# Optimization experiments

Measured on AMD Instinct MI355X. Metric: run time of the kernel, lower is better.

The kernel has to match this reference:

```python
import jax, jax.numpy as jnp
import numpy as np

N_STFT = 513
N_BARKS = 128
SAMPLE_RATE = 16000
F_MIN = 0.0
F_MAX = 8000.0
MAX_ITER = 30
TOL_LOSS = 1e-5
TOL_CHANGE = 1e-8
LR = 0.1
MOMENTUM = 0.9
BATCH = 4
TIME = 512


def _hz_to_bark(f):
    # traunmuller scale
    b = 26.81 * f / (1960.0 + f) - 0.53
    b = jnp.where(b < 2.0, b + 0.15 * (2.0 - b), b)
    b = jnp.where(b > 20.1, b + 0.22 * (b - 20.1), b)
    return b


def _bark_to_hz(b):
    b = jnp.where(b < 2.0, (b - 0.3) / 0.85, b)
    b = jnp.where(b > 20.1, (b + 4.422) / 1.22, b)
    return 1960.0 * (b + 0.53) / (26.28 - b)


def barkscale_fbanks():
    all_freqs = jnp.linspace(0.0, float(SAMPLE_RATE // 2), N_STFT)
    b_min = _hz_to_bark(jnp.float32(F_MIN))
    b_max = _hz_to_bark(jnp.float32(F_MAX))
    b_pts = jnp.linspace(b_min, b_max, N_BARKS + 2)
    f_pts = _bark_to_hz(b_pts)
    f_diff = f_pts[1:] - f_pts[:-1]                  # (n_barks+1,)
    slopes = f_pts[None, :] - all_freqs[:, None]     # (freq, n_barks+2)
    down = -slopes[:, :-2] / f_diff[:-1]
    up = slopes[:, 2:] / f_diff[1:]
    return jnp.maximum(0.0, jnp.minimum(down, up))   # (freq, n_barks)


def setup_inputs() -> dict:
    key = jax.random.key(0)
    k1, k2 = jax.random.split(key)
    barkspec = jax.random.uniform(k1, (BATCH, N_BARKS, TIME), dtype=jnp.float32)
    fb = barkscale_fbanks().astype(jnp.float32)                 # (freq, n_barks)
    spec_init = jax.random.uniform(k2, (BATCH, TIME, N_STFT), dtype=jnp.float32)
    return {"barkspec": barkspec, "fb": fb, "spec_init": spec_init}


def reference(barkspec, fb, spec_init):
    B, K, T = barkspec.shape
    m = jnp.swapaxes(barkspec, -1, -2)          # (B, T, n_barks)
    inv_n = 1.0 / (B * T)

    def step(carry, _):
        spec, buf, prev_loss, done = carry
        diff = m - jnp.einsum('btf,fk->btk', spec, fb)          # (B, T, K)
        loss = (diff * diff).sum(-1).mean()
        # closed-form grad of mean_{b,t} sum_k diff^2 wrt spec
        grad = (-2.0 * inv_n) * jnp.einsum('btk,fk->btf', diff, fb)
        # torch SGD with momentum, no dampening/nesterov
        buf_n = MOMENTUM * buf + grad
        spec_n = jnp.maximum(spec - LR * buf_n, 0.0)            # clamp(min=0)
        stop = (loss < TOL_LOSS) | (jnp.abs(prev_loss - loss) < TOL_CHANGE)
        spec = jnp.where(done, spec, spec_n)
        buf = jnp.where(done, buf, buf_n)
        prev = jnp.where(done, prev_loss, loss)
        return (spec, buf, prev, done | stop), None

    init = (spec_init, jnp.zeros_like(spec_init), jnp.float32(jnp.inf),
            jnp.array(False))
    (spec, _, _, _), _ = jax.lax.scan(step, init, None, length=MAX_ITER)
    return jnp.swapaxes(spec, -1, -2)           # (B, freq, T)
```

## Files before the change

### kernel.cpp

```cpp
#include <hip/hip_runtime.h>


#define NSTFT 513
#define NBARK 128
#define BATCH 4
#define TIME  512
#define MAXIT 30
#define NROWS (BATCH*TIME)
#define SA 6
#define SB 20

#define WS_S_OFF   0
#define WS_FT_OFF  256
#define WS_HA_OFF  8464
#define WS_HB_OFF  8976
#define WS_WT_OFF  9488
#define WS_BP_OFF  22800

__global__ __launch_bounds__(64) void setup_taps(const float* __restrict__ fb,
                                                 char* __restrict__ ws) {
    const int f = blockIdx.x, lane = threadIdx.x;
    const float2 v = ((const float2*)(fb + (size_t)f * NBARK))[lane];
    unsigned long long mx = __ballot(v.x > 0.f);
    unsigned long long my = __ballot(v.y > 0.f);
    int kx = mx ? 2 * (__ffsll(mx) - 1)     : 999;
    int ky = my ? 2 * (__ffsll(my) - 1) + 1 : 999;
    int k1 = min(kx, ky);
    float w1 = 0.f, w2 = 0.f;
    if (k1 < NBARK) {
        float sx = __shfl(v.x, k1 >> 1);
        float sy = __shfl(v.y, k1 >> 1);
        w1 = (k1 & 1) ? sy : sx;
        const int k2 = k1 + 1;
        if (k2 < NBARK) {
            float tx = __shfl(v.x, k2 >> 1);
            float ty = __shfl(v.y, k2 >> 1);
            w2 = (k2 & 1) ? ty : tx;
        }
    } else {
        k1 = (f < 256) ? 0 : 127;
    }
    if (lane == 0) {
        float4 e;
        e.x = __int_as_float(k1); e.y = w1;
        e.z = 0.f;                e.w = w2;
        ((float4*)(ws + WS_FT_OFF))[f] = e;
    }
}

__global__ __launch_bounds__(64) void setup_lanes(char* __restrict__ ws) {
    const int c = blockIdx.x, lane = threadIdx.x;
    const float4* ftab = (const float4*)(ws + WS_FT_OFF);
    int fmin = 0x7fffffff, fmax = -1;
    float4 e9[9];
#pragma unroll
    for (int s = 0; s < 9; ++s) {
        int f = lane + 64*s;
        e9[s] = (f < NSTFT) ? ftab[f] : make_float4(__int_as_float(-1),0,0,0);
        if (f < NSTFT && __float_as_int(e9[s].x) == c) {
            fmin = min(fmin, f); fmax = max(fmax, f);
        }
    }
#pragma unroll
    for (int m = 32; m; m >>= 1) {
        fmin = min(fmin, __shfl_xor(fmin, m));
        fmax = max(fmax, __shfl_xor(fmax, m));
    }
    int cnt = (fmax >= 0) ? (fmax - fmin + 1) : 0;
    if (fmax < 0) fmin = 0;
    const int cap  = (c < 64) ? SA : SB;
    const int base = (c < 64) ? 0  : SA;
    const int lf   = (c < 64) ? c  : 127 - c;
    cnt = min(cnt, cap);
    if (lane == 0)
        ((int2*)(ws + (c < 64 ? WS_HA_OFF : WS_HB_OFF)))[lf] =
            make_int2(fmin, cnt);
    if (lane < cap) {
        float2 wv = make_float2(0.f, 0.f);
        if (lane < cnt) {
            float4 e = ftab[fmin + lane];
            wv = make_float2(e.y, e.w);
        }
        ((float2*)(ws + WS_WT_OFF))[(base + lane)*64 + lf] = wv;
    }
}

__global__ __launch_bounds__(64, 2) void
iter_kernel(const float* __restrict__ barkspec,
            const float* __restrict__ spec_init,
            float* __restrict__ out,
            char* __restrict__ ws, int mode)
{
    const int lane = threadIdx.x;

    int niter = MAXIT;
    if (mode) {
        int S = *(const volatile int*)(ws + WS_S_OFF);
        if (S >= MAXIT) return;
        niter = S;
    }

    const int r     = blockIdx.x;
    const int batch = r >> 9;
    const int t     = r & (TIME - 1);

    const int2 hA = ((const int2*)(ws + WS_HA_OFF))[lane];
    const int2 hB = ((const int2*)(ws + WS_HB_OFF))[lane];
    const float2* wt = (const float2*)(ws + WS_WT_OFF);
    const float* spg = spec_init + ((size_t)batch*TIME + t)*NSTFT;

    float w1A[SA], w2A[SA], spA[SA], bfA[SA];
    float w1B[SB], w2B[SB], spB[SB], bfB[SB];
#pragma unroll
    for (int i = 0; i < SA; ++i) {
        float2 v = wt[i*64 + lane];
        w1A[i] = v.x; w2A[i] = v.y;
        spA[i] = (i < hA.y) ? spg[hA.x + i] : 0.f;
        bfA[i] = 0.f;
    }
#pragma unroll
    for (int i = 0; i < SB; ++i) {
        float2 v = wt[(SA + i)*64 + lane];
        w1B[i] = v.x; w2B[i] = v.y;
        spB[i] = (i < hB.y) ? spg[hB.x + i] : 0.f;
        bfB[i] = 0.f;
    }

    const float* bs = barkspec + (size_t)batch*NBARK*TIME + t;
    const float m0 = bs[(size_t)lane*TIME];
    const float m1 = bs[(size_t)(127 - lane)*TIME];

    float* bp = (float*)(ws + WS_BP_OFF);
    const float GC = -2.0f / (float)NROWS;

    float lp_prev = 0.f;

#pragma unroll 2
    for (int it = 0; it < niter; ++it) {
        float sBA = 0.f, sBB = 0.f;
#pragma unroll
        for (int i = 0; i < SA; ++i) sBA = fmaf(spA[i], w2A[i], sBA);
#pragma unroll
        for (int i = 0; i < SB; ++i) sBB = fmaf(spB[i], w2B[i], sBB);
        float cAin = __shfl_up(sBA, 1);
        float cBin = __shfl_down(sBB, 1);

        if (!mode && it > 0) {
            float lp = lp_prev;
#pragma unroll
            for (int m = 32; m; m >>= 1) lp += __shfl_xor(lp, m);
            if (lane == 0) bp[(it - 1)*NROWS + r] = lp;
        }

        float sAA = 0.f, sAB = 0.f;
#pragma unroll
        for (int i = 0; i < SA; ++i) sAA = fmaf(spA[i], w1A[i], sAA);
#pragma unroll
        for (int i = 0; i < SB; ++i) sAB = fmaf(spB[i], w1B[i], sAB);

        if (lane == 0)  cAin = 0.f;
        if (lane == 63) cBin = sBA;
        const float d0 = m0 - (sAA + cAin);
        const float d1 = m1 - (sAB + cBin);
        lp_prev = fmaf(d0, d0, d1*d1);

        float dAn = __shfl_down(d0, 1);
        float dBn = __shfl_up(d1, 1);
        const float g0 = GC * d0, g1 = GC * d1;
#pragma unroll
        for (int i = 0; i < SA; ++i) bfA[i] *= 0.9f;
#pragma unroll
        for (int i = 0; i < SB; ++i) bfB[i] *= 0.9f;
        if (lane == 63) dAn = d1;
        const float gA = GC * dAn, gB = GC * dBn;
#pragma unroll
        for (int i = 0; i < SA; ++i) {
            float g = fmaf(g0, w1A[i], gA * w2A[i]);
            bfA[i] += g;
            float v = fmaf(-0.1f, bfA[i], spA[i]);
            spA[i] = v < 0.f ? 0.f : v;
        }
#pragma unroll
        for (int i = 0; i < SB; ++i) {
            float g = fmaf(g1, w1B[i], gB * w2B[i]);
            bfB[i] += g;
            float v = fmaf(-0.1f, bfB[i], spB[i]);
            spB[i] = v < 0.f ? 0.f : v;
        }
    }

    if (!mode) {
        float lp = lp_prev;
#pragma unroll
        for (int m = 32; m; m >>= 1) lp += __shfl_xor(lp, m);
        if (lane == 0) bp[(niter - 1)*NROWS + r] = lp;
    }

    float* og = out + ((size_t)batch*NSTFT)*TIME + t;
#pragma unroll
    for (int i = 0; i < SA; ++i)
        if (i < hA.y) og[(size_t)(hA.x + i)*TIME] = spA[i];
#pragma unroll
    for (int i = 0; i < SB; ++i)
        if (i < hB.y) og[(size_t)(hB.x + i)*TIME] = spB[i];
}

__global__ __launch_bounds__(1024) void scan_all(char* __restrict__ ws) {
    __shared__ float losses[MAXIT];
    const int tid = threadIdx.x, wave = tid >> 6, lane = tid & 63;
    const float* bp = (const float*)(ws + WS_BP_OFF);
    for (int it = wave; it < MAXIT; it += 16) {
        const float4* b4 = (const float4*)(bp + (size_t)it*NROWS);
        float s = 0.f;
#pragma unroll
        for (int j = 0; j < NROWS/256; ++j) {
            float4 v = b4[j*64 + lane];
            s += (v.x + v.y) + (v.z + v.w);
        }
#pragma unroll
        for (int m = 32; m; m >>= 1) s += __shfl_xor(s, m);
        if (lane == 0) losses[it] = s * (1.0f/(float)NROWS);
    }
    __syncthreads();
    if (tid == 0) {
        float prev = __builtin_inff();
        int S = MAXIT;
        for (int i = 0; i < MAXIT; ++i) {
            float l = losses[i];
            if (l < 1e-5f || fabsf(prev - l) < 1e-8f) { S = i + 1; break; }
            prev = l;
        }
        *(int*)(ws + WS_S_OFF) = S;
    }
}

extern "C" void kernel_launch(void* const* d_in, const int* in_sizes, int n_in,
                              void* d_out, int out_size, void* d_ws, size_t ws_size,
                              hipStream_t stream)
{
    const float* barkspec  = (const float*)d_in[0];
    const float* fb        = (const float*)d_in[1];
    const float* spec_init = (const float*)d_in[2];
    float* out = (float*)d_out;
    char* ws = (char*)d_ws;

    setup_taps <<<NSTFT, 64, 0, stream>>>(fb, ws);
    setup_lanes<<<NBARK, 64, 0, stream>>>(ws);
    iter_kernel<<<NROWS, 64, 0, stream>>>(barkspec, spec_init, out, ws, 0);
    scan_all   <<<1, 1024, 0, stream>>>(ws);
    iter_kernel<<<NROWS, 64, 0, stream>>>(barkspec, spec_init, out, ws, 1);
}
```

Before: 104.9 us.

## Snapshot spectra every iteration and select the stop-step output instead of re-running

The main kernel now stores each row's spectrum to a workspace snapshot after every one of the 30 iterations, instead of writing the final output directly. The second iteration pass, which previously recomputed up to the early-stop step, is replaced by a select_out kernel that copies the snapshot for the chosen step into the transposed output. This removes the possible recomputation when early stopping triggers. In exchange it writes roughly 127 MB of snapshots per call and adds an extra transpose-copy kernel, even though the recompute pass exits immediately when no early stop occurs. The loop's unroll-by-2 pragma is also dropped.

```diff
diff --git a/kernel.cpp b/kernel.cpp
--- a/kernel.cpp
+++ b/kernel.cpp
@@ -9,13 +9,15 @@
 #define NROWS (BATCH*TIME)
 #define SA 6
 #define SB 20
-
-#define WS_S_OFF   0
-#define WS_FT_OFF  256
-#define WS_HA_OFF  8464
-#define WS_HB_OFF  8976
-#define WS_WT_OFF  9488
-#define WS_BP_OFF  22800
+#define ROWF 516
+
+#define WS_S_OFF    0
+#define WS_FT_OFF   256
+#define WS_HA_OFF   8464
+#define WS_HB_OFF   8976
+#define WS_WT_OFF   9488
+#define WS_BP_OFF   22800
+#define WS_SNAP_OFF 268800
 
 __global__ __launch_bounds__(64) void setup_taps(const float* __restrict__ fb,
                                                  char* __restrict__ ws) {
@@ -52,13 +54,12 @@
     const int c = blockIdx.x, lane = threadIdx.x;
     const float4* ftab = (const float4*)(ws + WS_FT_OFF);
     int fmin = 0x7fffffff, fmax = -1;
-    float4 e9[9];
 #pragma unroll
     for (int s = 0; s < 9; ++s) {
         int f = lane + 64*s;
-        e9[s] = (f < NSTFT) ? ftab[f] : make_float4(__int_as_float(-1),0,0,0);
-        if (f < NSTFT && __float_as_int(e9[s].x) == c) {
-            fmin = min(fmin, f); fmax = max(fmax, f);
+        if (f < NSTFT) {
+            float4 e = ftab[f];
+            if (__float_as_int(e.x) == c) { fmin = min(fmin, f); fmax = max(fmax, f); }
         }
     }
 #pragma unroll
@@ -86,19 +87,11 @@
 }
 
 __global__ __launch_bounds__(64, 2) void
-iter_kernel(const float* __restrict__ barkspec,
-            const float* __restrict__ spec_init,
-            float* __restrict__ out,
-            char* __restrict__ ws, int mode)
+iter_snap(const float* __restrict__ barkspec,
+          const float* __restrict__ spec_init,
+          char* __restrict__ ws)
 {
     const int lane = threadIdx.x;
-
-    int niter = MAXIT;
-    if (mode) {
-        int S = *(const volatile int*)(ws + WS_S_OFF);
-        if (S >= MAXIT) return;
-        niter = S;
-    }
 
     const int r     = blockIdx.x;
     const int batch = r >> 9;
@@ -131,12 +124,14 @@
     const float m1 = bs[(size_t)(127 - lane)*TIME];
 
     float* bp = (float*)(ws + WS_BP_OFF);
+    float* snA = (float*)(ws + WS_SNAP_OFF) + (size_t)r*ROWF + hA.x;
+    float* snB = (float*)(ws + WS_SNAP_OFF) + (size_t)r*ROWF + hB.x;
+    const size_t SNAP_IT = (size_t)NROWS * ROWF;
+
     const float GC = -2.0f / (float)NROWS;
-
     float lp_prev = 0.f;
 
-#pragma unroll 2
-    for (int it = 0; it < niter; ++it) {
+    for (int it = 0; it < MAXIT; ++it) {
         float sBA = 0.f, sBB = 0.f;
 #pragma unroll
         for (int i = 0; i < SA; ++i) sBA = fmaf(spA[i], w2A[i], sBA);
@@ -145,7 +140,7 @@
         float cAin = __shfl_up(sBA, 1);
         float cBin = __shfl_down(sBB, 1);
 
-        if (!mode && it > 0) {
+        if (it > 0) {
             float lp = lp_prev;
 #pragma unroll
             for (int m = 32; m; m >>= 1) lp += __shfl_xor(lp, m);
@@ -187,22 +182,22 @@
             float v = fmaf(-0.1f, bfB[i], spB[i]);
             spB[i] = v < 0.f ? 0.f : v;
         }
-    }
-
-    if (!mode) {
+
+#pragma unroll
+        for (int i = 0; i < SA; ++i)
+            if (i < hA.y) snA[i] = spA[i];
+#pragma unroll
+        for (int i = 0; i < SB; ++i)
+            if (i < hB.y) snB[i] = spB[i];
+        snA += SNAP_IT; snB += SNAP_IT;
+    }
+
+    {
         float lp = lp_prev;
 #pragma unroll
         for (int m = 32; m; m >>= 1) lp += __shfl_xor(lp, m);
-        if (lane == 0) bp[(niter - 1)*NROWS + r] = lp;
-    }
-
-    float* og = out + ((size_t)batch*NSTFT)*TIME + t;
-#pragma unroll
-    for (int i = 0; i < SA; ++i)
-        if (i < hA.y) og[(size_t)(hA.x + i)*TIME] = spA[i];
-#pragma unroll
-    for (int i = 0; i < SB; ++i)
-        if (i < hB.y) og[(size_t)(hB.x + i)*TIME] = spB[i];
+        if (lane == 0) bp[(MAXIT - 1)*NROWS + r] = lp;
+    }
 }
 
 __global__ __launch_bounds__(1024) void scan_all(char* __restrict__ ws) {
@@ -231,6 +226,26 @@
             prev = l;
         }
         *(int*)(ws + WS_S_OFF) = S;
+    }
+}
+
+__global__ __launch_bounds__(64) void select_out(const char* __restrict__ ws,
+                                                 float* __restrict__ out) {
+    const int lane = threadIdx.x;
+    const int S = *(const int*)(ws + WS_S_OFF);
+    const float* snap = (const float*)(ws + WS_SNAP_OFF)
+                      + (size_t)(S - 1) * NROWS * ROWF;
+    const int b  = blockIdx.x / 129;
+    const int f0 = (blockIdx.x % 129) * 4;
+    float* og = out + ((size_t)b*NSTFT + f0)*TIME;
+    for (int t0 = 0; t0 < TIME; t0 += 64) {
+        const int t = t0 + lane;
+        const int r = (b << 9) | t;
+        float4 v = *(const float4*)(snap + (size_t)r*ROWF + f0);
+        og[t] = v.x;
+        if (f0 + 1 < NSTFT) og[(size_t)TIME   + t] = v.y;
+        if (f0 + 2 < NSTFT) og[(size_t)2*TIME + t] = v.z;
+        if (f0 + 3 < NSTFT) og[(size_t)3*TIME + t] = v.w;
     }
 }
 
@@ -246,7 +261,7 @@
 
     setup_taps <<<NSTFT, 64, 0, stream>>>(fb, ws);
     setup_lanes<<<NBARK, 64, 0, stream>>>(ws);
-    iter_kernel<<<NROWS, 64, 0, stream>>>(barkspec, spec_init, out, ws, 0);
+    iter_snap  <<<NROWS, 64, 0, stream>>>(barkspec, spec_init, ws);
     scan_all   <<<1, 1024, 0, stream>>>(ws);
-    iter_kernel<<<NROWS, 64, 0, stream>>>(barkspec, spec_init, out, ws, 1);
-}
+    select_out <<<BATCH*129, 64, 0, stream>>>(ws, out);
+}
```

Result: slower. 170.4 us (+62.5%).

## Checkpoint optimizer state periodically and replay only the remaining iterations

Applied to the files above, without the earlier changes.

The first iteration kernel now always runs all 30 steps without writing the output. After steps 8, 16 and 24 it saves each row's spectrum and momentum registers to workspace. A new repair kernel reads the stop iteration S, restores the nearest checkpoint (or the initial state) and replays only the remaining steps before writing the output. The aim is to cap the redundant recompute for early stopping at fewer than eight iterations. In exchange it writes roughly 80 MB of checkpoints, and it always launches a repair pass that reloads state and reruns up to six steps, even when S is 30 and the old code could exit immediately.

```diff
diff --git a/kernel.cpp b/kernel.cpp
--- a/kernel.cpp
+++ b/kernel.cpp
@@ -9,6 +9,7 @@
 #define NROWS (BATCH*TIME)
 #define SA 6
 #define SB 20
+#define CPF  ((SA+SB)*64)
 
 #define WS_S_OFF   0
 #define WS_FT_OFF  256
@@ -16,6 +17,7 @@
 #define WS_HB_OFF  8976
 #define WS_WT_OFF  9488
 #define WS_BP_OFF  22800
+#define WS_CP_OFF  268800
 
 __global__ __launch_bounds__(64) void setup_taps(const float* __restrict__ fb,
                                                  char* __restrict__ ws) {
@@ -52,13 +54,12 @@
     const int c = blockIdx.x, lane = threadIdx.x;
     const float4* ftab = (const float4*)(ws + WS_FT_OFF);
     int fmin = 0x7fffffff, fmax = -1;
-    float4 e9[9];
 #pragma unroll
     for (int s = 0; s < 9; ++s) {
         int f = lane + 64*s;
-        e9[s] = (f < NSTFT) ? ftab[f] : make_float4(__int_as_float(-1),0,0,0);
-        if (f < NSTFT && __float_as_int(e9[s].x) == c) {
-            fmin = min(fmin, f); fmax = max(fmax, f);
+        if (f < NSTFT) {
+            float4 e = ftab[f];
+            if (__float_as_int(e.x) == c) { fmin = min(fmin, f); fmax = max(fmax, f); }
         }
     }
 #pragma unroll
@@ -86,20 +87,11 @@
 }
 
 __global__ __launch_bounds__(64, 2) void
-iter_kernel(const float* __restrict__ barkspec,
-            const float* __restrict__ spec_init,
-            float* __restrict__ out,
-            char* __restrict__ ws, int mode)
+iter_cp(const float* __restrict__ barkspec,
+        const float* __restrict__ spec_init,
+        char* __restrict__ ws)
 {
     const int lane = threadIdx.x;
-
-    int niter = MAXIT;
-    if (mode) {
-        int S = *(const volatile int*)(ws + WS_S_OFF);
-        if (S >= MAXIT) return;
-        niter = S;
-    }
-
     const int r     = blockIdx.x;
     const int batch = r >> 9;
     const int t     = r & (TIME - 1);
@@ -131,12 +123,11 @@
     const float m1 = bs[(size_t)(127 - lane)*TIME];
 
     float* bp = (float*)(ws + WS_BP_OFF);
+    float* cp = (float*)(ws + WS_CP_OFF);
     const float GC = -2.0f / (float)NROWS;
-
     float lp_prev = 0.f;
 
-#pragma unroll 2
-    for (int it = 0; it < niter; ++it) {
+    for (int it = 0; it < MAXIT; ++it) {
         float sBA = 0.f, sBB = 0.f;
 #pragma unroll
         for (int i = 0; i < SA; ++i) sBA = fmaf(spA[i], w2A[i], sBA);
@@ -145,7 +136,7 @@
         float cAin = __shfl_up(sBA, 1);
         float cBin = __shfl_down(sBB, 1);
 
-        if (!mode && it > 0) {
+        if (it > 0) {
             float lp = lp_prev;
 #pragma unroll
             for (int m = 32; m; m >>= 1) lp += __shfl_xor(lp, m);
@@ -187,22 +178,28 @@
             float v = fmaf(-0.1f, bfB[i], spB[i]);
             spB[i] = v < 0.f ? 0.f : v;
         }
-    }
-
-    if (!mode) {
+
+        if (it == 7 || it == 15 || it == 23) {
+            const int c = it >> 3;
+            float* cs = cp + ((size_t)(c*2 + 0)*NROWS + r)*CPF + lane;
+            float* cb = cp + ((size_t)(c*2 + 1)*NROWS + r)*CPF + lane;
+#pragma unroll
+            for (int i = 0; i < SA; ++i) {
+                cs[i*64] = spA[i];  cb[i*64] = bfA[i];
+            }
+#pragma unroll
+            for (int i = 0; i < SB; ++i) {
+                cs[(SA + i)*64] = spB[i];  cb[(SA + i)*64] = bfB[i];
+            }
+        }
+    }
+
+    {
         float lp = lp_prev;
 #pragma unroll
         for (int m = 32; m; m >>= 1) lp += __shfl_xor(lp, m);
-        if (lane == 0) bp[(niter - 1)*NROWS + r] = lp;
-    }
-
-    float* og = out + ((size_t)batch*NSTFT)*TIME + t;
-#pragma unroll
-    for (int i = 0; i < SA; ++i)
-        if (i < hA.y) og[(size_t)(hA.x + i)*TIME] = spA[i];
-#pragma unroll
-    for (int i = 0; i < SB; ++i)
-        if (i < hB.y) og[(size_t)(hB.x + i)*TIME] = spB[i];
+        if (lane == 0) bp[(MAXIT - 1)*NROWS + r] = lp;
+    }
 }
 
 __global__ __launch_bounds__(1024) void scan_all(char* __restrict__ ws) {
@@ -232,6 +229,122 @@
         }
         *(int*)(ws + WS_S_OFF) = S;
     }
+}
+
+__global__ __launch_bounds__(64) void
+repair_out(const float* __restrict__ barkspec,
+           const float* __restrict__ spec_init,
+           float* __restrict__ out,
+           const char* __restrict__ ws)
+{
+    const int lane = threadIdx.x;
+    const int r     = blockIdx.x;
+    const int batch = r >> 9;
+    const int t     = r & (TIME - 1);
+
+    const int S    = *(const int*)(ws + WS_S_OFF);
+    const int base = (S >= 24) ? 24 : (S >= 16) ? 16 : (S >= 8) ? 8 : 0;
+    const int R    = S - base;
+
+    const int2 hA = ((const int2*)(ws + WS_HA_OFF))[lane];
+    const int2 hB = ((const int2*)(ws + WS_HB_OFF))[lane];
+    const float2* wt = (const float2*)(ws + WS_WT_OFF);
+
+    float w1A[SA], w2A[SA], spA[SA], bfA[SA];
+    float w1B[SB], w2B[SB], spB[SB], bfB[SB];
+#pragma unroll
+    for (int i = 0; i < SA; ++i) {
+        float2 v = wt[i*64 + lane];
+        w1A[i] = v.x; w2A[i] = v.y;
+    }
+#pragma unroll
+    for (int i = 0; i < SB; ++i) {
+        float2 v = wt[(SA + i)*64 + lane];
+        w1B[i] = v.x; w2B[i] = v.y;
+    }
+
+    if (base == 0) {
+        const float* spg = spec_init + ((size_t)batch*TIME + t)*NSTFT;
+#pragma unroll
+        for (int i = 0; i < SA; ++i) {
+            spA[i] = (i < hA.y) ? spg[hA.x + i] : 0.f;  bfA[i] = 0.f;
+        }
+#pragma unroll
+        for (int i = 0; i < SB; ++i) {
+            spB[i] = (i < hB.y) ? spg[hB.x + i] : 0.f;  bfB[i] = 0.f;
+        }
+    } else {
+        const int c = (base >> 3) - 1;
+        const float* cp = (const float*)(ws + WS_CP_OFF);
+        const float* cs = cp + ((size_t)(c*2 + 0)*NROWS + r)*CPF + lane;
+        const float* cb = cp + ((size_t)(c*2 + 1)*NROWS + r)*CPF + lane;
+#pragma unroll
+        for (int i = 0; i < SA; ++i) {
+            spA[i] = cs[i*64];  bfA[i] = cb[i*64];
+        }
+#pragma unroll
+        for (int i = 0; i < SB; ++i) {
+            spB[i] = cs[(SA + i)*64];  bfB[i] = cb[(SA + i)*64];
+        }
+    }
+
+    const float* bs = barkspec + (size_t)batch*NBARK*TIME + t;
+    const float m0 = bs[(size_t)lane*TIME];
+    const float m1 = bs[(size_t)(127 - lane)*TIME];
+    const float GC = -2.0f / (float)NROWS;
+
+    for (int it = 0; it < R; ++it) {
+        float sBA = 0.f, sBB = 0.f;
+#pragma unroll
+        for (int i = 0; i < SA; ++i) sBA = fmaf(spA[i], w2A[i], sBA);
+#pragma unroll
+        for (int i = 0; i < SB; ++i) sBB = fmaf(spB[i], w2B[i], sBB);
+        float cAin = __shfl_up(sBA, 1);
+        float cBin = __shfl_down(sBB, 1);
+
+        float sAA = 0.f, sAB = 0.f;
+#pragma unroll
+        for (int i = 0; i < SA; ++i) sAA = fmaf(spA[i], w1A[i], sAA);
+#pragma unroll
+        for (int i = 0; i < SB; ++i) sAB = fmaf(spB[i], w1B[i], sAB);
+
+        if (lane == 0)  cAin = 0.f;
+        if (lane == 63) cBin = sBA;
+        const float d0 = m0 - (sAA + cAin);
+        const float d1 = m1 - (sAB + cBin);
+
+        float dAn = __shfl_down(d0, 1);
+        float dBn = __shfl_up(d1, 1);
+        const float g0 = GC * d0, g1 = GC * d1;
+#pragma unroll
+        for (int i = 0; i < SA; ++i) bfA[i] *= 0.9f;
+#pragma unroll
+        for (int i = 0; i < SB; ++i) bfB[i] *= 0.9f;
+        if (lane == 63) dAn = d1;
+        const float gA = GC * dAn, gB = GC * dBn;
+#pragma unroll
+        for (int i = 0; i < SA; ++i) {
+            float g = fmaf(g0, w1A[i], gA * w2A[i]);
+            bfA[i] += g;
+            float v = fmaf(-0.1f, bfA[i], spA[i]);
+            spA[i] = v < 0.f ? 0.f : v;
+        }
+#pragma unroll
+        for (int i = 0; i < SB; ++i) {
+            float g = fmaf(g1, w1B[i], gB * w2B[i]);
+            bfB[i] += g;
+            float v = fmaf(-0.1f, bfB[i], spB[i]);
+            spB[i] = v < 0.f ? 0.f : v;
+        }
+    }
+
+    float* og = out + ((size_t)batch*NSTFT)*TIME + t;
+#pragma unroll
+    for (int i = 0; i < SA; ++i)
+        if (i < hA.y) og[(size_t)(hA.x + i)*TIME] = spA[i];
+#pragma unroll
+    for (int i = 0; i < SB; ++i)
+        if (i < hB.y) og[(size_t)(hB.x + i)*TIME] = spB[i];
 }
 
 extern "C" void kernel_launch(void* const* d_in, const int* in_sizes, int n_in,
@@ -246,7 +359,7 @@
 
     setup_taps <<<NSTFT, 64, 0, stream>>>(fb, ws);
     setup_lanes<<<NBARK, 64, 0, stream>>>(ws);
-    iter_kernel<<<NROWS, 64, 0, stream>>>(barkspec, spec_init, out, ws, 0);
+    iter_cp    <<<NROWS, 64, 0, stream>>>(barkspec, spec_init, ws);
     scan_all   <<<1, 1024, 0, stream>>>(ws);
-    iter_kernel<<<NROWS, 64, 0, stream>>>(barkspec, spec_init, out, ws, 1);
-}
+    repair_out <<<NROWS, 64, 0, stream>>>(barkspec, spec_init, out, ws);
+}
```

Measured after the change: 121.2 us. 1.16x slower.

## Store per-lane losses, reduce in a multi-block kernel, scan in iter kernel

Applied to the files above, without the earlier changes.

Each iteration now writes per-lane squared errors straight to workspace, so the per-iteration wave shuffle reduction in the solver loop goes away. The single-block scan is replaced by a 30-block reduce kernel that sums each iteration's losses in parallel. The stop-iteration scan moves into the second solver pass, where every block recomputes it. The dot products are split into two accumulators to shorten dependency chains. The price is 64x more loss traffic to memory (about 15 MB written and then read back).

```diff
diff --git a/kernel.cpp b/kernel.cpp
--- a/kernel.cpp
+++ b/kernel.cpp
@@ -10,12 +10,12 @@
 #define SA 6
 #define SB 20
 
-#define WS_S_OFF   0
+#define WS_L_OFF   16
 #define WS_FT_OFF  256
 #define WS_HA_OFF  8464
 #define WS_HB_OFF  8976
 #define WS_WT_OFF  9488
-#define WS_BP_OFF  22800
+#define WS_BP_OFF  22848
 
 __global__ __launch_bounds__(64) void setup_taps(const float* __restrict__ fb,
                                                  char* __restrict__ ws) {
@@ -52,13 +52,12 @@
     const int c = blockIdx.x, lane = threadIdx.x;
     const float4* ftab = (const float4*)(ws + WS_FT_OFF);
     int fmin = 0x7fffffff, fmax = -1;
-    float4 e9[9];
 #pragma unroll
     for (int s = 0; s < 9; ++s) {
         int f = lane + 64*s;
-        e9[s] = (f < NSTFT) ? ftab[f] : make_float4(__int_as_float(-1),0,0,0);
-        if (f < NSTFT && __float_as_int(e9[s].x) == c) {
-            fmin = min(fmin, f); fmax = max(fmax, f);
+        if (f < NSTFT) {
+            float4 e = ftab[f];
+            if (__float_as_int(e.x) == c) { fmin = min(fmin, f); fmax = max(fmax, f); }
         }
     }
 #pragma unroll
@@ -95,134 +94,7 @@
 
     int niter = MAXIT;
     if (mode) {
-        int S = *(const volatile int*)(ws + WS_S_OFF);
-        if (S >= MAXIT) return;
-        niter = S;
-    }
-
-    const int r     = blockIdx.x;
-    const int batch = r >> 9;
-    const int t     = r & (TIME - 1);
-
-    const int2 hA = ((const int2*)(ws + WS_HA_OFF))[lane];
-    const int2 hB = ((const int2*)(ws + WS_HB_OFF))[lane];
-    const float2* wt = (const float2*)(ws + WS_WT_OFF);
-    const float* spg = spec_init + ((size_t)batch*TIME + t)*NSTFT;
-
-    float w1A[SA], w2A[SA], spA[SA], bfA[SA];
-    float w1B[SB], w2B[SB], spB[SB], bfB[SB];
-#pragma unroll
-    for (int i = 0; i < SA; ++i) {
-        float2 v = wt[i*64 + lane];
-        w1A[i] = v.x; w2A[i] = v.y;
-        spA[i] = (i < hA.y) ? spg[hA.x + i] : 0.f;
-        bfA[i] = 0.f;
-    }
-#pragma unroll
-    for (int i = 0; i < SB; ++i) {
-        float2 v = wt[(SA + i)*64 + lane];
-        w1B[i] = v.x; w2B[i] = v.y;
-        spB[i] = (i < hB.y) ? spg[hB.x + i] : 0.f;
-        bfB[i] = 0.f;
-    }
-
-    const float* bs = barkspec + (size_t)batch*NBARK*TIME + t;
-    const float m0 = bs[(size_t)lane*TIME];
-    const float m1 = bs[(size_t)(127 - lane)*TIME];
-
-    float* bp = (float*)(ws + WS_BP_OFF);
-    const float GC = -2.0f / (float)NROWS;
-
-    float lp_prev = 0.f;
-
-#pragma unroll 2
-    for (int it = 0; it < niter; ++it) {
-        float sBA = 0.f, sBB = 0.f;
-#pragma unroll
-        for (int i = 0; i < SA; ++i) sBA = fmaf(spA[i], w2A[i], sBA);
-#pragma unroll
-        for (int i = 0; i < SB; ++i) sBB = fmaf(spB[i], w2B[i], sBB);
-        float cAin = __shfl_up(sBA, 1);
-        float cBin = __shfl_down(sBB, 1);
-
-        if (!mode && it > 0) {
-            float lp = lp_prev;
-#pragma unroll
-            for (int m = 32; m; m >>= 1) lp += __shfl_xor(lp, m);
-            if (lane == 0) bp[(it - 1)*NROWS + r] = lp;
-        }
-
-        float sAA = 0.f, sAB = 0.f;
-#pragma unroll
-        for (int i = 0; i < SA; ++i) sAA = fmaf(spA[i], w1A[i], sAA);
-#pragma unroll
-        for (int i = 0; i < SB; ++i) sAB = fmaf(spB[i], w1B[i], sAB);
-
-        if (lane == 0)  cAin = 0.f;
-        if (lane == 63) cBin = sBA;
-        const float d0 = m0 - (sAA + cAin);
-        const float d1 = m1 - (sAB + cBin);
-        lp_prev = fmaf(d0, d0, d1*d1);
-
-        float dAn = __shfl_down(d0, 1);
-        float dBn = __shfl_up(d1, 1);
-        const float g0 = GC * d0, g1 = GC * d1;
-#pragma unroll
-        for (int i = 0; i < SA; ++i) bfA[i] *= 0.9f;
-#pragma unroll
-        for (int i = 0; i < SB; ++i) bfB[i] *= 0.9f;
-        if (lane == 63) dAn = d1;
-        const float gA = GC * dAn, gB = GC * dBn;
-#pragma unroll
-        for (int i = 0; i < SA; ++i) {
-            float g = fmaf(g0, w1A[i], gA * w2A[i]);
-            bfA[i] += g;
-            float v = fmaf(-0.1f, bfA[i], spA[i]);
-            spA[i] = v < 0.f ? 0.f : v;
-        }
-#pragma unroll
-        for (int i = 0; i < SB; ++i) {
-            float g = fmaf(g1, w1B[i], gB * w2B[i]);
-            bfB[i] += g;
-            float v = fmaf(-0.1f, bfB[i], spB[i]);
-            spB[i] = v < 0.f ? 0.f : v;
-        }
-    }
-
-    if (!mode) {
-        float lp = lp_prev;
-#pragma unroll
-        for (int m = 32; m; m >>= 1) lp += __shfl_xor(lp, m);
-        if (lane == 0) bp[(niter - 1)*NROWS + r] = lp;
-    }
-
-    float* og = out + ((size_t)batch*NSTFT)*TIME + t;
-#pragma unroll
-    for (int i = 0; i < SA; ++i)
-        if (i < hA.y) og[(size_t)(hA.x + i)*TIME] = spA[i];
-#pragma unroll
-    for (int i = 0; i < SB; ++i)
-        if (i < hB.y) og[(size_t)(hB.x + i)*TIME] = spB[i];
-}
-
-__global__ __launch_bounds__(1024) void scan_all(char* __restrict__ ws) {
-    __shared__ float losses[MAXIT];
-    const int tid = threadIdx.x, wave = tid >> 6, lane = tid & 63;
-    const float* bp = (const float*)(ws + WS_BP_OFF);
-    for (int it = wave; it < MAXIT; it += 16) {
-        const float4* b4 = (const float4*)(bp + (size_t)it*NROWS);
-        float s = 0.f;
-#pragma unroll
-        for (int j = 0; j < NROWS/256; ++j) {
-            float4 v = b4[j*64 + lane];
-            s += (v.x + v.y) + (v.z + v.w);
-        }
-#pragma unroll
-        for (int m = 32; m; m >>= 1) s += __shfl_xor(s, m);
-        if (lane == 0) losses[it] = s * (1.0f/(float)NROWS);
-    }
-    __syncthreads();
-    if (tid == 0) {
+        const float* losses = (const float*)(ws + WS_L_OFF);
         float prev = __builtin_inff();
         int S = MAXIT;
         for (int i = 0; i < MAXIT; ++i) {
@@ -230,7 +102,127 @@
             if (l < 1e-5f || fabsf(prev - l) < 1e-8f) { S = i + 1; break; }
             prev = l;
         }
-        *(int*)(ws + WS_S_OFF) = S;
+        if (S >= MAXIT) return;
+        niter = S;
+    }
+
+    const int r     = blockIdx.x;
+    const int batch = r >> 9;
+    const int t     = r & (TIME - 1);
+
+    const int2 hA = ((const int2*)(ws + WS_HA_OFF))[lane];
+    const int2 hB = ((const int2*)(ws + WS_HB_OFF))[lane];
+    const float2* wt = (const float2*)(ws + WS_WT_OFF);
+    const float* spg = spec_init + ((size_t)batch*TIME + t)*NSTFT;
+
+    float w1A[SA], w2A[SA], spA[SA], bfA[SA];
+    float w1B[SB], w2B[SB], spB[SB], bfB[SB];
+#pragma unroll
+    for (int i = 0; i < SA; ++i) {
+        float2 v = wt[i*64 + lane];
+        w1A[i] = v.x; w2A[i] = v.y;
+        spA[i] = (i < hA.y) ? spg[hA.x + i] : 0.f;
+        bfA[i] = 0.f;
+    }
+#pragma unroll
+    for (int i = 0; i < SB; ++i) {
+        float2 v = wt[(SA + i)*64 + lane];
+        w1B[i] = v.x; w2B[i] = v.y;
+        spB[i] = (i < hB.y) ? spg[hB.x + i] : 0.f;
+        bfB[i] = 0.f;
+    }
+
+    const float* bs = barkspec + (size_t)batch*NBARK*TIME + t;
+    const float m0 = bs[(size_t)lane*TIME];
+    const float m1 = bs[(size_t)(127 - lane)*TIME];
+
+    float* bpL = (float*)(ws + WS_BP_OFF) + (size_t)r*64 + lane;
+    const float GC = -2.0f / (float)NROWS;
+
+    for (int it = 0; it < niter; ++it) {
+        float sBA = 0.f, sBB0 = 0.f, sBB1 = 0.f;
+#pragma unroll
+        for (int i = 0; i < SA; ++i) sBA = fmaf(spA[i], w2A[i], sBA);
+#pragma unroll
+        for (int i = 0; i < SB/2; ++i) sBB0 = fmaf(spB[i], w2B[i], sBB0);
+#pragma unroll
+        for (int i = SB/2; i < SB; ++i) sBB1 = fmaf(spB[i], w2B[i], sBB1);
+        const float sBB = sBB0 + sBB1;
+        float cAin = __shfl_up(sBA, 1);
+        float cBin = __shfl_down(sBB, 1);
+
+        float sAA = 0.f, sAB0 = 0.f, sAB1 = 0.f;
+#pragma unroll
+        for (int i = 0; i < SA; ++i) sAA = fmaf(spA[i], w1A[i], sAA);
+#pragma unroll
+        for (int i = 0; i < SB/2; ++i) sAB0 = fmaf(spB[i], w1B[i], sAB0);
+#pragma unroll
+        for (int i = SB/2; i < SB; ++i) sAB1 = fmaf(spB[i], w1B[i], sAB1);
+        const float sAB = sAB0 + sAB1;
+
+        if (lane == 0)  cAin = 0.f;
+        if (lane == 63) cBin = sBA;
+        const float d0 = m0 - (sAA + cAin);
+        const float d1 = m1 - (sAB + cBin);
+
+        if (!mode) { bpL[0] = fmaf(d0, d0, d1*d1); bpL += NROWS*64; }
+
+        float dAn = __shfl_down(d0, 1);
+        float dBn = __shfl_up(d1, 1);
+        const float g0 = GC * d0, g1 = GC * d1;
+#pragma unroll
+        for (int i = 0; i < SA; ++i) bfA[i] *= 0.9f;
+#pragma unroll
+        for (int i = 0; i < SB; ++i) bfB[i] *= 0.9f;
+        if (lane == 63) dAn = d1;
+        const float gA = GC * dAn, gB = GC * dBn;
+#pragma unroll
+        for (int i = 0; i < SA; ++i) {
+            float g = fmaf(g0, w1A[i], gA * w2A[i]);
+            bfA[i] += g;
+            float v = fmaf(-0.1f, bfA[i], spA[i]);
+            spA[i] = v < 0.f ? 0.f : v;
+        }
+#pragma unroll
+        for (int i = 0; i < SB; ++i) {
+            float g = fmaf(g1, w1B[i], gB * w2B[i]);
+            bfB[i] += g;
+            float v = fmaf(-0.1f, bfB[i], spB[i]);
+            spB[i] = v < 0.f ? 0.f : v;
+        }
+    }
+
+    float* og = out + ((size_t)batch*NSTFT)*TIME + t;
+#pragma unroll
+    for (int i = 0; i < SA; ++i)
+        if (i < hA.y) og[(size_t)(hA.x + i)*TIME] = spA[i];
+#pragma unroll
+    for (int i = 0; i < SB; ++i)
+        if (i < hB.y) og[(size_t)(hB.x + i)*TIME] = spB[i];
+}
+
+__global__ __launch_bounds__(1024) void scan_reduce(char* __restrict__ ws) {
+    __shared__ float wsum[16];
+    const int it = blockIdx.x, tid = threadIdx.x;
+    const int wave = tid >> 6, lane = tid & 63;
+    const float4* b4 = (const float4*)((const float*)(ws + WS_BP_OFF)
+                                       + (size_t)it*NROWS*64);
+    float s = 0.f;
+#pragma unroll
+    for (int j = 0; j < 32; ++j) {
+        float4 v = b4[tid + j*1024];
+        s += (v.x + v.y) + (v.z + v.w);
+    }
+#pragma unroll
+    for (int m = 32; m; m >>= 1) s += __shfl_xor(s, m);
+    if (lane == 0) wsum[wave] = s;
+    __syncthreads();
+    if (wave == 0) {
+        float v = (lane < 16) ? wsum[lane] : 0.f;
+#pragma unroll
+        for (int m = 8; m; m >>= 1) v += __shfl_xor(v, m);
+        if (lane == 0)
+            ((float*)(ws + WS_L_OFF))[it] = v * (1.0f/(float)NROWS);
     }
 }
 
@@ -247,6 +239,6 @@
     setup_taps <<<NSTFT, 64, 0, stream>>>(fb, ws);
     setup_lanes<<<NBARK, 64, 0, stream>>>(ws);
     iter_kernel<<<NROWS, 64, 0, stream>>>(barkspec, spec_init, out, ws, 0);
-    scan_all   <<<1, 1024, 0, stream>>>(ws);
+    scan_reduce<<<MAXIT, 1024, 0, stream>>>(ws);
     iter_kernel<<<NROWS, 64, 0, stream>>>(barkspec, spec_init, out, ws, 1);
 }
```

After: 109.3 us. +4.2%, slower.
